# Kernel optimization log

Hardware: AMD Instinct MI355X
Metric: run time of the kernel (lower is better)

The kernel has to match this reference:

```python
import math
import jax, jax.numpy as jnp
import numpy as np

B, S, E, A, H, L, V = 4, 1024, 1024, 64, 16, 2, 32000
EPS = 1e-5
SCALE = math.sqrt(E)  # torch code scales by sqrt(input_dim) = sqrt(embedding_dim)
W_INIT_SCALE = 0.05   # torch.rand is U[0,1); scaled down for numerically sane softmax


def setup_inputs() -> dict:
    key = jax.random.key(0)
    ks = jax.random.split(key, 6)
    return {
        "x": jax.random.randint(ks[0], (B, S), 0, V),
        "emb": jax.random.normal(ks[1], (V, E), dtype=jnp.float32) * 0.02,
        "ln_gamma": jnp.ones((L, E), dtype=jnp.float32),
        "ln_beta": jnp.zeros((L, E), dtype=jnp.float32),
        "Wq": jax.random.uniform(ks[2], (L, H, A, E), dtype=jnp.float32) * W_INIT_SCALE,
        "Wk": jax.random.uniform(ks[3], (L, H, A, E), dtype=jnp.float32) * W_INIT_SCALE,
        "Wv": jax.random.uniform(ks[4], (L, H, E, E), dtype=jnp.float32) * W_INIT_SCALE,
    }


def _attn_layer(h, gamma, beta, wq, wk, wv):
    # h: [B,H,S,E]; LayerNorm over last dim (biased variance, like torch)
    mu = jnp.mean(h, axis=-1, keepdims=True)
    var = jnp.mean(jnp.square(h - mu), axis=-1, keepdims=True)
    hn = (h - mu) * jax.lax.rsqrt(var + EPS) * gamma + beta
    q = jnp.einsum('bhse,hae->bhsa', hn, wq)   # [B,H,S,A]
    k = jnp.einsum('bhse,hae->bhsa', hn, wk)   # [B,H,S,A]
    v = jnp.einsum('bhse,hoe->bhso', hn, wv)   # [B,H,S,E]
    scores = jnp.einsum('bhsa,bhta->bhst', q, k) / SCALE  # [B,H,S,S]
    w = jax.nn.softmax(scores, axis=-1)
    return jnp.einsum('bhst,bhto->bhso', w, v)  # [B,H,S,E]


def reference(x, emb, ln_gamma, ln_beta, Wq, Wk, Wv):
    # embed then replicate across heads: [B,S,E] -> [B,H,S,E]
    h = jnp.broadcast_to(emb[x][:, None, :, :], (B, H, S, E))
    for l in range(L):
        h = _attn_layer(h, ln_gamma[l], ln_beta[l], Wq[l], Wk[l], Wv[l])
    return h
```

## Files before the change

### kernel.cpp

```cpp
#include <hip/hip_runtime.h>

#define B_ 4
#define S_ 1024
#define E_ 1024
#define A_ 64
#define H_ 16
#define L_ 2

static constexpr float LN_EPS = 1e-5f;
static constexpr float INV_SCALE = 1.0f / 32.0f;

typedef __attribute__((ext_vector_type(8))) short bf16x8;
typedef __attribute__((ext_vector_type(4))) float f32x4;

__device__ __forceinline__ unsigned short f2bf(float f) {
  unsigned u = __float_as_uint(f);
  u += 0x7fffu + ((u >> 16) & 1u);
  return (unsigned short)(u >> 16);
}
__device__ __forceinline__ float bf2f(unsigned short s) {
  return __uint_as_float(((unsigned)s) << 16);
}

__device__ __forceinline__ float block_sum256(float v, float* red) {
#pragma unroll
  for (int o = 32; o > 0; o >>= 1) v += __shfl_down(v, o, 64);
  const int lane = threadIdx.x & 63;
  const int w = threadIdx.x >> 6;
  if (lane == 0) red[w] = v;
  __syncthreads();
  if (threadIdx.x == 0) red[0] = red[0] + red[1] + red[2] + red[3];
  __syncthreads();
  float r = red[0];
  __syncthreads();
  return r;
}

__global__ __launch_bounds__(256) void cvt_f32_bf16(const float* __restrict__ in,
                                                    unsigned short* __restrict__ out, long n) {
  long i = ((long)blockIdx.x * 256 + threadIdx.x) * 4;
  const long stride = (long)gridDim.x * 1024;
  for (; i < n; i += stride) {
    float4 v = *(const float4*)(in + i);
    ushort4 o;
    o.x = f2bf(v.x); o.y = f2bf(v.y); o.z = f2bf(v.z); o.w = f2bf(v.w);
    *(ushort4*)(out + i) = o;
  }
}

__global__ __launch_bounds__(256) void cvt_qk_concat(const float* __restrict__ Wq,
                                                     const float* __restrict__ Wk,
                                                     unsigned short* __restrict__ out) {
  const long total = (long)L_ * H_ * 128 * E_;
  long i = ((long)blockIdx.x * 256 + threadIdx.x) * 4;
  const long stride = (long)gridDim.x * 1024;
  for (; i < total; i += stride) {
    const long e = i % E_;
    const long rowhe = i / E_;
    const int row = (int)(rowhe % 128);
    const long lh = rowhe / 128;
    const float* src = (row < 64 ? Wq : Wk) + (lh * 64 + (row & 63)) * E_ + e;
    float4 v = *(const float4*)src;
    ushort4 o;
    o.x = f2bf(v.x); o.y = f2bf(v.y); o.z = f2bf(v.z); o.w = f2bf(v.w);
    *(ushort4*)(out + i) = o;
  }
}

__global__ __launch_bounds__(256) void embed_ln_kernel(
    const int* __restrict__ x, const float* __restrict__ emb,
    const float* __restrict__ gamma, const float* __restrict__ beta,
    unsigned short* __restrict__ out) {
  __shared__ float red[4];
  const int row = blockIdx.x;
  const int tid = threadIdx.x;
  const float* src = emb + (long)x[row] * E_;
  float4 v = *(const float4*)(src + tid * 4);
  const float mean = block_sum256(v.x + v.y + v.z + v.w, red) * (1.f / E_);
  float dx = v.x - mean, dy = v.y - mean, dz = v.z - mean, dw = v.w - mean;
  const float var = block_sum256(dx * dx + dy * dy + dz * dz + dw * dw, red) * (1.f / E_);
  const float rstd = rsqrtf(var + LN_EPS);
  float4 g = *(const float4*)(gamma + tid * 4);
  float4 b = *(const float4*)(beta + tid * 4);
  ushort4 o;
  o.x = f2bf(dx * rstd * g.x + b.x);
  o.y = f2bf(dy * rstd * g.y + b.y);
  o.z = f2bf(dz * rstd * g.z + b.z);
  o.w = f2bf(dw * rstd * g.w + b.w);
  *(ushort4*)(out + (long)row * E_ + tid * 4) = o;
}

__global__ __launch_bounds__(256) void ln_bf16_kernel(
    const unsigned short* __restrict__ h, const float* __restrict__ gamma,
    const float* __restrict__ beta, unsigned short* __restrict__ out) {
  __shared__ float red[4];
  const long row = blockIdx.x;
  const int tid = threadIdx.x;
  ushort4 raw = *(const ushort4*)(h + row * (long)E_ + tid * 4);
  float vx = bf2f(raw.x), vy = bf2f(raw.y), vz = bf2f(raw.z), vw = bf2f(raw.w);
  const float mean = block_sum256(vx + vy + vz + vw, red) * (1.f / E_);
  float dx = vx - mean, dy = vy - mean, dz = vz - mean, dw = vw - mean;
  const float var = block_sum256(dx * dx + dy * dy + dz * dz + dw * dw, red) * (1.f / E_);
  const float rstd = rsqrtf(var + LN_EPS);
  float4 g = *(const float4*)(gamma + tid * 4);
  float4 b = *(const float4*)(beta + tid * 4);
  ushort4 o;
  o.x = f2bf(dx * rstd * g.x + b.x);
  o.y = f2bf(dy * rstd * g.y + b.y);
  o.z = f2bf(dz * rstd * g.z + b.z);
  o.w = f2bf(dw * rstd * g.w + b.w);
  *(ushort4*)(out + row * E_ + tid * 4) = o;
}

__device__ __forceinline__ void gload_lds16(const void* g, void* l) {
  __builtin_amdgcn_global_load_lds((const __attribute__((address_space(1))) void*)g,
                                   (__attribute__((address_space(3))) void*)l, 16, 0, 0);
}

template <int ROWS>
__device__ __forceinline__ void stage_tile(const unsigned short* __restrict__ src, int ldRow,
                                           unsigned short* lds, int tid) {
  const int rb = tid >> 3;
  const int gslot = (tid & 7) ^ (rb & 7);
  const int wbase = (tid >> 6) * 512;
#pragma unroll
  for (int i = 0; i < ROWS / 32; ++i) {
    const unsigned short* g = src + (long)(i * 32 + rb) * ldRow + gslot * 8;
    gload_lds16(g, lds + i * 2048 + wbase);
  }
}

__device__ __forceinline__ bf16x8 lds_frag(const unsigned short* base, int r, int slot) {
  const int byteoff = (r << 7) + ((slot ^ (r & 7)) << 4);
  return *(const bf16x8*)((const char*)base + byteoff);
}

template <int BM, int BN, bool OUT_BF16>
__global__ __launch_bounds__(256) void mfma_gemm_nt(
    const unsigned short* __restrict__ Aall, const unsigned short* __restrict__ Ball,
    void* __restrict__ Call, int M, int N, int K, int lda, int ldb,
    long aSB, long aSH, long bSB, long bSH, int Hn, float alpha) {
  __shared__ unsigned short As[BM * 64];
  __shared__ unsigned short Bs[BN * 64];
  const int batch = blockIdx.z;
  const int bb = batch / Hn, hh = batch % Hn;
  const unsigned short* Ap = Aall + (long)bb * aSB + (long)hh * aSH;
  const unsigned short* Bp = Ball + (long)bb * bSB + (long)hh * bSH;
  const int tid = threadIdx.x;
  const int lane = tid & 63;
  const int wave = tid >> 6;
  const int wr = wave >> 1, wc = wave & 1;
  const int bm = blockIdx.x * BM, bn = blockIdx.y * BN;
  constexpr int FM = BM / 32, FN = BN / 32;

  f32x4 acc[FM][FN];
#pragma unroll
  for (int i = 0; i < FM; ++i)
#pragma unroll
    for (int j = 0; j < FN; ++j) acc[i][j] = (f32x4)(0.f);

  for (int k0 = 0; k0 < K; k0 += 64) {
    stage_tile<BM>(Ap + (long)bm * lda + k0, lda, As, tid);
    stage_tile<BN>(Bp + (long)bn * ldb + k0, ldb, Bs, tid);
    __syncthreads();
#pragma unroll
    for (int kb = 0; kb < 2; ++kb) {
      const int slot = (kb << 2) + (lane >> 4);
      bf16x8 af[FM], bfv[FN];
#pragma unroll
      for (int mi = 0; mi < FM; ++mi)
        af[mi] = lds_frag(As, wr * (BM / 2) + mi * 16 + (lane & 15), slot);
#pragma unroll
      for (int ni = 0; ni < FN; ++ni)
        bfv[ni] = lds_frag(Bs, wc * (BN / 2) + ni * 16 + (lane & 15), slot);
#pragma unroll
      for (int mi = 0; mi < FM; ++mi)
#pragma unroll
        for (int ni = 0; ni < FN; ++ni)
          acc[mi][ni] = __builtin_amdgcn_mfma_f32_16x16x32_bf16(af[mi], bfv[ni], acc[mi][ni], 0, 0, 0);
    }
    __syncthreads();
  }

#pragma unroll
  for (int mi = 0; mi < FM; ++mi) {
    const int row = bm + wr * (BM / 2) + mi * 16 + ((lane >> 4) << 2);
#pragma unroll
    for (int ni = 0; ni < FN; ++ni) {
      const int col = bn + wc * (BN / 2) + ni * 16 + (lane & 15);
#pragma unroll
      for (int r = 0; r < 4; ++r) {
        const float v = acc[mi][ni][r] * alpha;
        const long idx = (long)batch * M * N + (long)(row + r) * N + col;
        if constexpr (OUT_BF16)
          ((unsigned short*)Call)[idx] = f2bf(v);
        else
          ((float*)Call)[idx] = v;
      }
    }
  }
}

__device__ __forceinline__ void stage_unit256(const unsigned short* __restrict__ src, int ldRow,
                                              char* lds_unit, int tid) {
#pragma unroll
  for (int i = 0; i < 2; ++i) {
    const int r = i * 128 + (tid >> 2);
    const int sg = (tid & 3) ^ ((r >> 1) & 3);
    const unsigned short* g = src + (long)r * ldRow + sg * 8;
    gload_lds16(g, lds_unit + i * 8192 + ((tid >> 6) << 10));
  }
}

__device__ __forceinline__ bf16x8 lds_frag256(const char* opbase, int kh, int r, int ss) {
  return *(const bf16x8*)(opbase + kh * 16384 + r * 64 + ((ss ^ ((r >> 1) & 3)) << 4));
}

template <bool OUT_BF16>
__global__ __launch_bounds__(512) void mfma_gemm256_nt(
    const unsigned short* __restrict__ Aall, const unsigned short* __restrict__ Ball,
    void* __restrict__ Call, int M, int N, int K, int lda, int ldb,
    long aSB, long aSH, long bSB, long bSH, int Hn, float alpha) {
  extern __shared__ char lds[];
  const int nx = gridDim.x, ny = gridDim.y;
  const int nwg = nx * ny * gridDim.z;
  int f = blockIdx.x + nx * (blockIdx.y + ny * blockIdx.z);
  if ((nwg & 7) == 0) f = (f & 7) * (nwg >> 3) + (f >> 3);
  const int bx = f % nx;
  const int by = (f / nx) % ny;
  const int batch = f / (nx * ny);

  const int bb = batch / Hn, hh = batch % Hn;
  const unsigned short* Ap = Aall + (long)bb * aSB + (long)hh * aSH + (long)bx * 256 * lda;
  const unsigned short* Bp = Ball + (long)bb * bSB + (long)hh * bSH + (long)by * 256 * ldb;
  const int tid = threadIdx.x;
  const int lane = tid & 63;
  const int w = tid >> 6;
  const int wr = w >> 2, wc = w & 3;
  const int ss = lane >> 4;
  const int ar = lane & 15;

  f32x4 acc[8][4];
#pragma unroll
  for (int i = 0; i < 8; ++i)
#pragma unroll
    for (int j = 0; j < 4; ++j) acc[i][j] = (f32x4)(0.f);

  const int NT = K >> 6;
  stage_unit256(Ap, lda, lds, tid);
  stage_unit256(Ap + 32, lda, lds + 16384, tid);
  stage_unit256(Bp, ldb, lds + 32768, tid);
  stage_unit256(Bp + 32, ldb, lds + 49152, tid);
  __syncthreads();

  for (int t = 0; t < NT; ++t) {
    const char* cur = lds + (t & 1) * 65536;
    char* nxt = lds + ((t + 1) & 1) * 65536;
    if (t + 1 < NT) {
      const unsigned short* An = Ap + (long)(t + 1) * 64;
      const unsigned short* Bn = Bp + (long)(t + 1) * 64;
      stage_unit256(An, lda, nxt, tid);
      stage_unit256(An + 32, lda, nxt + 16384, tid);
      stage_unit256(Bn, ldb, nxt + 32768, tid);
      stage_unit256(Bn + 32, ldb, nxt + 49152, tid);
    }
#pragma unroll
    for (int kh = 0; kh < 2; ++kh) {
      bf16x8 b[4], a[8];
#pragma unroll
      for (int ni = 0; ni < 4; ++ni)
        b[ni] = lds_frag256(cur + 32768, kh, wc * 64 + ni * 16 + ar, ss);
#pragma unroll
      for (int mi = 0; mi < 8; ++mi)
        a[mi] = lds_frag256(cur, kh, wr * 128 + mi * 16 + ar, ss);
#pragma unroll
      for (int mi = 0; mi < 8; ++mi)
#pragma unroll
        for (int ni = 0; ni < 4; ++ni)
          acc[mi][ni] = __builtin_amdgcn_mfma_f32_16x16x32_bf16(a[mi], b[ni], acc[mi][ni], 0, 0, 0);
    }
    __syncthreads();
  }

#pragma unroll
  for (int mi = 0; mi < 8; ++mi) {
    const int row0 = bx * 256 + wr * 128 + mi * 16 + ((lane >> 4) << 2);
#pragma unroll
    for (int ni = 0; ni < 4; ++ni) {
      const int col = by * 256 + wc * 64 + ni * 16 + (lane & 15);
#pragma unroll
      for (int r = 0; r < 4; ++r) {
        const float v = acc[mi][ni][r] * alpha;
        const long idx = (long)batch * M * N + (long)(row0 + r) * N + col;
        if constexpr (OUT_BF16)
          ((unsigned short*)Call)[idx] = f2bf(v);
        else
          ((float*)Call)[idx] = v;
      }
    }
  }
}

__global__ __launch_bounds__(512) void scores_softmax_kernel(
    const unsigned short* __restrict__ qk, unsigned short* __restrict__ sc) {
  extern __shared__ char smem[];
  unsigned short* q_lds = (unsigned short*)smem;
  unsigned short* k_lds = (unsigned short*)(smem + 8192);
  float* redm = (float*)(smem + 8192 + 131072);
  float* reds = redm + 512;

  const int tid = threadIdx.x;
  const int lane = tid & 63;
  const int w = tid >> 6;
  const int batch = blockIdx.z;
  const int bm = blockIdx.x * 64;
  const unsigned short* qbase = qk + (long)batch * S_ * 128 + (long)bm * 128;
  const unsigned short* kbase = qk + (long)batch * S_ * 128 + 64;

  {
    const int r = tid >> 3;
    const int slot = (tid & 7) ^ (r & 7);
    gload_lds16(qbase + (long)r * 128 + slot * 8, (char*)q_lds + w * 1024);
  }
#pragma unroll
  for (int p = 0; p < 16; ++p) {
    const int r = p * 64 + (tid >> 3);
    const int slot = (tid & 7) ^ (r & 7);
    gload_lds16(kbase + (long)r * 128 + slot * 8, (char*)k_lds + p * 8192 + w * 1024);
  }
  __syncthreads();

  const int ss = lane >> 4, ar = lane & 15;
  f32x4 acc[4][8];
#pragma unroll
  for (int i = 0; i < 4; ++i)
#pragma unroll
    for (int j = 0; j < 8; ++j) acc[i][j] = (f32x4)(0.f);

#pragma unroll
  for (int kh = 0; kh < 2; ++kh) {
    bf16x8 a[4];
#pragma unroll
    for (int mi = 0; mi < 4; ++mi)
      a[mi] = lds_frag(q_lds, mi * 16 + ar, kh * 4 + ss);
#pragma unroll
    for (int ni = 0; ni < 8; ++ni) {
      bf16x8 bv = lds_frag(k_lds, w * 128 + ni * 16 + ar, kh * 4 + ss);
#pragma unroll
      for (int mi = 0; mi < 4; ++mi)
        acc[mi][ni] = __builtin_amdgcn_mfma_f32_16x16x32_bf16(a[mi], bv, acc[mi][ni], 0, 0, 0);
    }
  }

#pragma unroll
  for (int mi = 0; mi < 4; ++mi)
#pragma unroll
    for (int ni = 0; ni < 8; ++ni)
#pragma unroll
      for (int r = 0; r < 4; ++r) acc[mi][ni][r] *= INV_SCALE;

  float gmax[4][4];
#pragma unroll
  for (int mi = 0; mi < 4; ++mi)
#pragma unroll
    for (int r = 0; r < 4; ++r) {
      float m = acc[mi][0][r];
#pragma unroll
      for (int ni = 1; ni < 8; ++ni) m = fmaxf(m, acc[mi][ni][r]);
#pragma unroll
      for (int mask = 1; mask < 16; mask <<= 1) m = fmaxf(m, __shfl_xor(m, mask, 64));
      if ((lane & 15) == 0) redm[(mi * 16 + (lane >> 4) * 4 + r) * 8 + w] = m;
      gmax[mi][r] = m;
    }
  __syncthreads();
#pragma unroll
  for (int mi = 0; mi < 4; ++mi)
#pragma unroll
    for (int r = 0; r < 4; ++r) {
      const int row = mi * 16 + (lane >> 4) * 4 + r;
      float g = redm[row * 8];
#pragma unroll
      for (int w2 = 1; w2 < 8; ++w2) g = fmaxf(g, redm[row * 8 + w2]);
      gmax[mi][r] = g;
    }

  float ginv[4][4];
#pragma unroll
  for (int mi = 0; mi < 4; ++mi)
#pragma unroll
    for (int r = 0; r < 4; ++r) {
      float s = 0.f;
#pragma unroll
      for (int ni = 0; ni < 8; ++ni) {
        const float e = __expf(acc[mi][ni][r] - gmax[mi][r]);
        acc[mi][ni][r] = e;
        s += e;
      }
#pragma unroll
      for (int mask = 1; mask < 16; mask <<= 1) s += __shfl_xor(s, mask, 64);
      if ((lane & 15) == 0) reds[(mi * 16 + (lane >> 4) * 4 + r) * 8 + w] = s;
    }
  __syncthreads();
#pragma unroll
  for (int mi = 0; mi < 4; ++mi)
#pragma unroll
    for (int r = 0; r < 4; ++r) {
      const int row = mi * 16 + (lane >> 4) * 4 + r;
      float g = 0.f;
#pragma unroll
      for (int w2 = 0; w2 < 8; ++w2) g += reds[row * 8 + w2];
      ginv[mi][r] = 1.f / g;
    }

  unsigned short* out = sc + (long)batch * S_ * S_;
#pragma unroll
  for (int mi = 0; mi < 4; ++mi)
#pragma unroll
    for (int r = 0; r < 4; ++r) {
      const long row = bm + mi * 16 + (lane >> 4) * 4 + r;
#pragma unroll
      for (int ni = 0; ni < 8; ++ni) {
        const int col = w * 128 + ni * 16 + ar;
        out[row * S_ + col] = f2bf(acc[mi][ni][r] * ginv[mi][r]);
      }
    }
}

extern "C" void kernel_launch(void* const* d_in, const int* in_sizes, int n_in,
                              void* d_out, int out_size, void* d_ws, size_t ws_size,
                              hipStream_t stream) {
  const int* x = (const int*)d_in[0];
  const float* emb = (const float*)d_in[1];
  const float* gamma = (const float*)d_in[2];
  const float* beta = (const float*)d_in[3];
  const float* Wq = (const float*)d_in[4];
  const float* Wk = (const float*)d_in[5];
  const float* Wv = (const float*)d_in[6];
  float* out = (float*)d_out;

  (void)hipFuncSetAttribute(reinterpret_cast<const void*>(&mfma_gemm256_nt<true>),
                            hipFuncAttributeMaxDynamicSharedMemorySize, 131072);
  (void)hipFuncSetAttribute(reinterpret_cast<const void*>(&mfma_gemm256_nt<false>),
                            hipFuncAttributeMaxDynamicSharedMemorySize, 131072);
  (void)hipFuncSetAttribute(reinterpret_cast<const void*>(&scores_softmax_kernel),
                            hipFuncAttributeMaxDynamicSharedMemorySize, 143360);

  const long WQK_N = (long)L_ * H_ * 128 * E_;
  const long WV_N = (long)L_ * H_ * E_ * E_;
  const long HN_N = (long)B_ * H_ * S_ * E_;
  const long QK_N = (long)B_ * H_ * S_ * 128;
  unsigned short* wqk = (unsigned short*)d_ws;
  unsigned short* wv_bf = wqk + WQK_N;
  unsigned short* hn = wv_bf + WV_N;
  unsigned short* qk = hn + HN_N;
  unsigned short* v_t = qk + QK_N;
  unsigned short* sc = v_t + HN_N;
  unsigned short* hid0 = (unsigned short*)d_out;

  const dim3 blk(256), blk512(512);
  const dim3 grid256(4, 4, 64);
  cvt_qk_concat<<<2048, blk, 0, stream>>>(Wq, Wk, wqk);
  cvt_f32_bf16<<<4096, blk, 0, stream>>>(Wv, wv_bf, WV_N);

  for (int l = 0; l < L_; ++l) {
    long hSB, hSH;
    if (l == 0) {
      embed_ln_kernel<<<B_ * S_, blk, 0, stream>>>(x, emb, gamma, beta, hn);
      hSB = (long)S_ * E_; hSH = 0;
    } else {
      ln_bf16_kernel<<<B_ * H_ * S_, blk, 0, stream>>>(
          hid0, gamma + (long)l * E_, beta + (long)l * E_, hn);
      hSB = (long)H_ * S_ * E_; hSH = (long)S_ * E_;
    }
    mfma_gemm_nt<128, 128, true><<<dim3(8, 1, 64), blk, 0, stream>>>(
        hn, wqk + (long)l * H_ * 128 * E_, qk, S_, 128, E_, E_, E_,
        hSB, hSH, 0L, (long)128 * E_, H_, 1.f);
    mfma_gemm256_nt<true><<<grid256, blk512, 131072, stream>>>(
        wv_bf + (long)l * H_ * E_ * E_, hn, v_t, E_, S_, E_, E_, E_,
        0L, (long)E_ * E_, hSB, hSH, H_, 1.f);
    scores_softmax_kernel<<<dim3(16, 1, 64), blk512, 143360, stream>>>(qk, sc);
    if (l == 0) {
      mfma_gemm256_nt<true><<<grid256, blk512, 131072, stream>>>(
          sc, v_t, hid0, S_, E_, S_, S_, S_,
          (long)H_ * S_ * S_, (long)S_ * S_, (long)H_ * E_ * S_, (long)E_ * S_, H_, 1.f);
    } else {
      mfma_gemm256_nt<false><<<grid256, blk512, 131072, stream>>>(
          sc, v_t, out, S_, E_, S_, S_, S_,
          (long)H_ * S_ * S_, (long)S_ * S_, (long)H_ * E_ * S_, (long)E_ * S_, H_, 1.f);
    }
  }
}
```

Measured before the change: 1.031 ms.

## Interleave GEMM loads with MFMA phases and stage bf16 outputs through LDS

The 256x256 GEMM main loop is split into four phases. Each phase issues one quarter of the next tile's global-to-LDS prefetch, waits with explicit vmcnt/lgkmcnt and barriers, and then runs a 4x4 MFMA block at raised wave priority. The goal is to overlap memory traffic with matrix math more evenly and keep fewer fragments live in registers, with launch bounds now requesting two blocks. Both bf16-output paths, the GEMM epilogue and the softmax kernel, now stage results in LDS and write 16-byte vectorized rows instead of scattered 2-byte stores. The cost is extra barriers and hand-tuned wait counts that could be fragile.

New measurement: 1.051 ms. Within noise of the previous version (+1.9%).

```diff
diff --git a/kernel.cpp b/kernel.cpp
--- a/kernel.cpp
+++ b/kernel.cpp
@@ -12,6 +12,8 @@
 
 typedef __attribute__((ext_vector_type(8))) short bf16x8;
 typedef __attribute__((ext_vector_type(4))) float f32x4;
+
+#define SCHED0 __builtin_amdgcn_sched_barrier(0)
 
 __device__ __forceinline__ unsigned short f2bf(float f) {
   unsigned u = __float_as_uint(f);
@@ -217,7 +219,7 @@
 }
 
 template <bool OUT_BF16>
-__global__ __launch_bounds__(512) void mfma_gemm256_nt(
+__global__ __launch_bounds__(512, 2) void mfma_gemm256_nt(
     const unsigned short* __restrict__ Aall, const unsigned short* __restrict__ Ball,
     void* __restrict__ Call, int M, int N, int K, int lda, int ldb,
     long aSB, long aSH, long bSB, long bSH, int Hn, float alpha) {
@@ -248,54 +250,143 @@
 
   const int NT = K >> 6;
   stage_unit256(Ap, lda, lds, tid);
+  stage_unit256(Bp, ldb, lds + 32768, tid);
   stage_unit256(Ap + 32, lda, lds + 16384, tid);
-  stage_unit256(Bp, ldb, lds + 32768, tid);
   stage_unit256(Bp + 32, ldb, lds + 49152, tid);
-  __syncthreads();
+  asm volatile("s_waitcnt vmcnt(4)");
+  SCHED0;
+  __builtin_amdgcn_s_barrier();
+  SCHED0;
 
   for (int t = 0; t < NT; ++t) {
     const char* cur = lds + (t & 1) * 65536;
     char* nxt = lds + ((t + 1) & 1) * 65536;
-    if (t + 1 < NT) {
-      const unsigned short* An = Ap + (long)(t + 1) * 64;
-      const unsigned short* Bn = Bp + (long)(t + 1) * 64;
-      stage_unit256(An, lda, nxt, tid);
+    const unsigned short* An = Ap + (long)(t + 1) * 64;
+    const unsigned short* Bn = Bp + (long)(t + 1) * 64;
+    const bool pf = (t + 1 < NT);
+    bf16x8 a[4], b[4];
+
+#pragma unroll
+    for (int ni = 0; ni < 4; ++ni)
+      b[ni] = lds_frag256(cur + 32768, 0, wc * 64 + ni * 16 + ar, ss);
+#pragma unroll
+    for (int mi = 0; mi < 4; ++mi)
+      a[mi] = lds_frag256(cur, 0, wr * 128 + mi * 16 + ar, ss);
+    if (pf) stage_unit256(An, lda, nxt, tid);
+    asm volatile("s_waitcnt vmcnt(4)");
+    SCHED0;
+    __builtin_amdgcn_s_barrier();
+    asm volatile("s_waitcnt lgkmcnt(0)");
+    SCHED0;
+    __builtin_amdgcn_s_setprio(1);
+#pragma unroll
+    for (int mi = 0; mi < 4; ++mi)
+#pragma unroll
+      for (int ni = 0; ni < 4; ++ni)
+        acc[mi][ni] = __builtin_amdgcn_mfma_f32_16x16x32_bf16(a[mi], b[ni], acc[mi][ni], 0, 0, 0);
+    __builtin_amdgcn_s_setprio(0);
+    __builtin_amdgcn_s_barrier();
+    SCHED0;
+
+#pragma unroll
+    for (int mi = 0; mi < 4; ++mi)
+      a[mi] = lds_frag256(cur, 0, wr * 128 + 64 + mi * 16 + ar, ss);
+    if (pf) stage_unit256(Bn, ldb, nxt + 32768, tid);
+    asm volatile("s_waitcnt vmcnt(4)");
+    SCHED0;
+    __builtin_amdgcn_s_barrier();
+    asm volatile("s_waitcnt lgkmcnt(0)");
+    SCHED0;
+    __builtin_amdgcn_s_setprio(1);
+#pragma unroll
+    for (int mi = 0; mi < 4; ++mi)
+#pragma unroll
+      for (int ni = 0; ni < 4; ++ni)
+        acc[4 + mi][ni] = __builtin_amdgcn_mfma_f32_16x16x32_bf16(a[mi], b[ni], acc[4 + mi][ni], 0, 0, 0);
+    __builtin_amdgcn_s_setprio(0);
+    __builtin_amdgcn_s_barrier();
+    SCHED0;
+
+#pragma unroll
+    for (int ni = 0; ni < 4; ++ni)
+      b[ni] = lds_frag256(cur + 32768, 1, wc * 64 + ni * 16 + ar, ss);
+#pragma unroll
+    for (int mi = 0; mi < 4; ++mi)
+      a[mi] = lds_frag256(cur, 1, wr * 128 + mi * 16 + ar, ss);
+    if (pf) {
       stage_unit256(An + 32, lda, nxt + 16384, tid);
-      stage_unit256(Bn, ldb, nxt + 32768, tid);
-      stage_unit256(Bn + 32, ldb, nxt + 49152, tid);
-    }
-#pragma unroll
-    for (int kh = 0; kh < 2; ++kh) {
-      bf16x8 b[4], a[8];
+      asm volatile("s_waitcnt vmcnt(4)");
+    } else {
+      asm volatile("s_waitcnt vmcnt(0)");
+    }
+    SCHED0;
+    __builtin_amdgcn_s_barrier();
+    asm volatile("s_waitcnt lgkmcnt(0)");
+    SCHED0;
+    __builtin_amdgcn_s_setprio(1);
+#pragma unroll
+    for (int mi = 0; mi < 4; ++mi)
 #pragma unroll
       for (int ni = 0; ni < 4; ++ni)
-        b[ni] = lds_frag256(cur + 32768, kh, wc * 64 + ni * 16 + ar, ss);
-#pragma unroll
-      for (int mi = 0; mi < 8; ++mi)
-        a[mi] = lds_frag256(cur, kh, wr * 128 + mi * 16 + ar, ss);
-#pragma unroll
-      for (int mi = 0; mi < 8; ++mi)
-#pragma unroll
-        for (int ni = 0; ni < 4; ++ni)
-          acc[mi][ni] = __builtin_amdgcn_mfma_f32_16x16x32_bf16(a[mi], b[ni], acc[mi][ni], 0, 0, 0);
-    }
+        acc[mi][ni] = __builtin_amdgcn_mfma_f32_16x16x32_bf16(a[mi], b[ni], acc[mi][ni], 0, 0, 0);
+    __builtin_amdgcn_s_setprio(0);
+    __builtin_amdgcn_s_barrier();
+    SCHED0;
+
+#pragma unroll
+    for (int mi = 0; mi < 4; ++mi)
+      a[mi] = lds_frag256(cur, 1, wr * 128 + 64 + mi * 16 + ar, ss);
+    if (pf) stage_unit256(Bn + 32, ldb, nxt + 49152, tid);
+    asm volatile("s_waitcnt vmcnt(4)");
+    SCHED0;
+    __builtin_amdgcn_s_barrier();
+    asm volatile("s_waitcnt lgkmcnt(0)");
+    SCHED0;
+    __builtin_amdgcn_s_setprio(1);
+#pragma unroll
+    for (int mi = 0; mi < 4; ++mi)
+#pragma unroll
+      for (int ni = 0; ni < 4; ++ni)
+        acc[4 + mi][ni] = __builtin_amdgcn_mfma_f32_16x16x32_bf16(a[mi], b[ni], acc[4 + mi][ni], 0, 0, 0);
+    __builtin_amdgcn_s_setprio(0);
+    __builtin_amdgcn_s_barrier();
+    SCHED0;
+  }
+
+  if constexpr (OUT_BF16) {
     __syncthreads();
-  }
-
-#pragma unroll
-  for (int mi = 0; mi < 8; ++mi) {
-    const int row0 = bx * 256 + wr * 128 + mi * 16 + ((lane >> 4) << 2);
-#pragma unroll
-    for (int ni = 0; ni < 4; ++ni) {
-      const int col = by * 256 + wc * 64 + ni * 16 + (lane & 15);
-#pragma unroll
-      for (int r = 0; r < 4; ++r) {
-        const float v = acc[mi][ni][r] * alpha;
-        const long idx = (long)batch * M * N + (long)(row0 + r) * N + col;
-        if constexpr (OUT_BF16)
-          ((unsigned short*)Call)[idx] = f2bf(v);
-        else
-          ((float*)Call)[idx] = v;
+    char* wbuf = lds + w * 16384;
+#pragma unroll
+    for (int mi = 0; mi < 8; ++mi)
+#pragma unroll
+      for (int ni = 0; ni < 4; ++ni)
+#pragma unroll
+        for (int r = 0; r < 4; ++r) {
+          const int rl = mi * 16 + ((lane >> 4) << 2) + r;
+          const int cl = ni * 16 + ar;
+          *(unsigned short*)(wbuf + rl * 128 + cl * 2) = f2bf(acc[mi][ni][r] * alpha);
+        }
+    unsigned short* Cb = (unsigned short*)Call + (long)batch * M * N;
+    const int R0 = bx * 256 + wr * 128, C0 = by * 256 + wc * 64;
+#pragma unroll
+    for (int it = 0; it < 16; ++it) {
+      const int row = it * 8 + (lane >> 3);
+      const int colc = (lane & 7) * 8;
+      bf16x8 v = *(const bf16x8*)(wbuf + row * 128 + colc * 2);
+      *(bf16x8*)(Cb + (long)(R0 + row) * N + C0 + colc) = v;
+    }
+  } else {
+#pragma unroll
+    for (int mi = 0; mi < 8; ++mi) {
+      const int row0 = bx * 256 + wr * 128 + mi * 16 + ((lane >> 4) << 2);
+#pragma unroll
+      for (int ni = 0; ni < 4; ++ni) {
+        const int col = by * 256 + wc * 64 + ni * 16 + ar;
+#pragma unroll
+        for (int r = 0; r < 4; ++r) {
+          const long idx = (long)batch * M * N + (long)(row0 + r) * N + col;
+          ((float*)Call)[idx] = acc[mi][ni][r] * alpha;
+        }
       }
     }
   }
@@ -412,18 +503,28 @@
       ginv[mi][r] = 1.f / g;
     }
 
-  unsigned short* out = sc + (long)batch * S_ * S_;
+  __syncthreads();
 #pragma unroll
   for (int mi = 0; mi < 4; ++mi)
 #pragma unroll
     for (int r = 0; r < 4; ++r) {
-      const long row = bm + mi * 16 + (lane >> 4) * 4 + r;
+      const int row = mi * 16 + (lane >> 4) * 4 + r;
 #pragma unroll
       for (int ni = 0; ni < 8; ++ni) {
         const int col = w * 128 + ni * 16 + ar;
-        out[row * S_ + col] = f2bf(acc[mi][ni][r] * ginv[mi][r]);
+        *(unsigned short*)((char*)k_lds + row * 2048 + col * 2) =
+            f2bf(acc[mi][ni][r] * ginv[mi][r]);
       }
     }
+  __syncthreads();
+  unsigned short* outp = sc + (long)batch * S_ * S_;
+#pragma unroll
+  for (int it = 0; it < 16; ++it) {
+    const int row = it * 4 + (tid >> 7);
+    const int colc = (tid & 127) * 8;
+    bf16x8 v = *(const bf16x8*)((char*)k_lds + row * 2048 + colc * 2);
+    *(bf16x8*)(outp + (long)(bm + row) * S_ + colc) = v;
+  }
 }
 
 extern "C" void kernel_launch(void* const* d_in, const int* in_sizes, int n_in,
```

## Interleave GEMM prefetch with MFMA phases using fine-grained barriers and priority

Applied to the files above, without the earlier changes.

Splits each K-tile of the 256x256 bf16 GEMM into four phases. Each phase loads half the A fragments, issues one staged global-to-LDS load for the next tile, and runs a block of MFMAs under raised wave priority. Partial vmcnt waits and raw s_barriers replace the single __syncthreads, so global loads overlap with compute. It also sets launch_bounds occupancy to 2 blocks per CU. The risks are more barriers per tile, possible register pressure, and correctness that depends on hand-counted vmcnt values.

Result: faster. 0.9998 ms (-3.1%).

```diff
diff --git a/kernel.cpp b/kernel.cpp
--- a/kernel.cpp
+++ b/kernel.cpp
@@ -217,7 +217,7 @@
 }
 
 template <bool OUT_BF16>
-__global__ __launch_bounds__(512) void mfma_gemm256_nt(
+__global__ __launch_bounds__(512, 2) void mfma_gemm256_nt(
     const unsigned short* __restrict__ Aall, const unsigned short* __restrict__ Ball,
     void* __restrict__ Call, int M, int N, int K, int lda, int ldb,
     long aSB, long aSH, long bSB, long bSH, int Hn, float alpha) {
@@ -248,38 +248,85 @@
 
   const int NT = K >> 6;
   stage_unit256(Ap, lda, lds, tid);
+  stage_unit256(Bp, ldb, lds + 32768, tid);
   stage_unit256(Ap + 32, lda, lds + 16384, tid);
-  stage_unit256(Bp, ldb, lds + 32768, tid);
   stage_unit256(Bp + 32, ldb, lds + 49152, tid);
-  __syncthreads();
+  asm volatile("s_waitcnt vmcnt(4)\n\ts_barrier" ::: "memory");
 
   for (int t = 0; t < NT; ++t) {
     const char* cur = lds + (t & 1) * 65536;
     char* nxt = lds + ((t + 1) & 1) * 65536;
-    if (t + 1 < NT) {
-      const unsigned short* An = Ap + (long)(t + 1) * 64;
-      const unsigned short* Bn = Bp + (long)(t + 1) * 64;
-      stage_unit256(An, lda, nxt, tid);
-      stage_unit256(An + 32, lda, nxt + 16384, tid);
-      stage_unit256(Bn, ldb, nxt + 32768, tid);
+    const unsigned short* An = Ap + (long)(t + 1) * 64;
+    const unsigned short* Bn = Bp + (long)(t + 1) * 64;
+    const bool pf = (t + 1 < NT);
+    bf16x8 a[4], b[4];
+
+#pragma unroll
+    for (int ni = 0; ni < 4; ++ni)
+      b[ni] = lds_frag256(cur + 32768, 0, wc * 64 + ni * 16 + ar, ss);
+#pragma unroll
+    for (int mi = 0; mi < 4; ++mi)
+      a[mi] = lds_frag256(cur, 0, wr * 128 + mi * 16 + ar, ss);
+    if (pf) stage_unit256(An, lda, nxt, tid);
+    asm volatile("s_barrier" ::: "memory");
+    __builtin_amdgcn_s_setprio(1);
+#pragma unroll
+    for (int mi = 0; mi < 4; ++mi)
+#pragma unroll
+      for (int ni = 0; ni < 4; ++ni)
+        acc[mi][ni] = __builtin_amdgcn_mfma_f32_16x16x32_bf16(a[mi], b[ni], acc[mi][ni], 0, 0, 0);
+    __builtin_amdgcn_s_setprio(0);
+    asm volatile("s_barrier" ::: "memory");
+
+#pragma unroll
+    for (int mi = 0; mi < 4; ++mi)
+      a[mi] = lds_frag256(cur, 0, wr * 128 + 64 + mi * 16 + ar, ss);
+    if (pf) stage_unit256(Bn, ldb, nxt + 32768, tid);
+    if (pf) asm volatile("s_waitcnt vmcnt(4)\n\ts_barrier" ::: "memory");
+    else    asm volatile("s_waitcnt vmcnt(0)\n\ts_barrier" ::: "memory");
+    __builtin_amdgcn_s_setprio(1);
+#pragma unroll
+    for (int mi = 0; mi < 4; ++mi)
+#pragma unroll
+      for (int ni = 0; ni < 4; ++ni)
+        acc[4 + mi][ni] = __builtin_amdgcn_mfma_f32_16x16x32_bf16(a[mi], b[ni], acc[4 + mi][ni], 0, 0, 0);
+    __builtin_amdgcn_s_setprio(0);
+    asm volatile("s_barrier" ::: "memory");
+
+#pragma unroll
+    for (int ni = 0; ni < 4; ++ni)
+      b[ni] = lds_frag256(cur + 32768, 1, wc * 64 + ni * 16 + ar, ss);
+#pragma unroll
+    for (int mi = 0; mi < 4; ++mi)
+      a[mi] = lds_frag256(cur, 1, wr * 128 + mi * 16 + ar, ss);
+    if (pf) stage_unit256(An + 32, lda, nxt + 16384, tid);
+    asm volatile("s_barrier" ::: "memory");
+    __builtin_amdgcn_s_setprio(1);
+#pragma unroll
+    for (int mi = 0; mi < 4; ++mi)
+#pragma unroll
+      for (int ni = 0; ni < 4; ++ni)
+        acc[mi][ni] = __builtin_amdgcn_mfma_f32_16x16x32_bf16(a[mi], b[ni], acc[mi][ni], 0, 0, 0);
+    __builtin_amdgcn_s_setprio(0);
+    asm volatile("s_barrier" ::: "memory");
+
+#pragma unroll
+    for (int mi = 0; mi < 4; ++mi)
+      a[mi] = lds_frag256(cur, 1, wr * 128 + 64 + mi * 16 + ar, ss);
+    if (pf) {
       stage_unit256(Bn + 32, ldb, nxt + 49152, tid);
-    }
-#pragma unroll
-    for (int kh = 0; kh < 2; ++kh) {
-      bf16x8 b[4], a[8];
+      asm volatile("s_waitcnt vmcnt(4)\n\ts_barrier" ::: "memory");
+    } else {
+      asm volatile("s_barrier" ::: "memory");
+    }
+    __builtin_amdgcn_s_setprio(1);
+#pragma unroll
+    for (int mi = 0; mi < 4; ++mi)
 #pragma unroll
       for (int ni = 0; ni < 4; ++ni)
-        b[ni] = lds_frag256(cur + 32768, kh, wc * 64 + ni * 16 + ar, ss);
-#pragma unroll
-      for (int mi = 0; mi < 8; ++mi)
-        a[mi] = lds_frag256(cur, kh, wr * 128 + mi * 16 + ar, ss);
-#pragma unroll
-      for (int mi = 0; mi < 8; ++mi)
-#pragma unroll
-        for (int ni = 0; ni < 4; ++ni)
-          acc[mi][ni] = __builtin_amdgcn_mfma_f32_16x16x32_bf16(a[mi], b[ni], acc[mi][ni], 0, 0, 0);
-    }
-    __syncthreads();
+        acc[4 + mi][ni] = __builtin_amdgcn_mfma_f32_16x16x32_bf16(a[mi], b[ni], acc[4 + mi][ni], 0, 0, 0);
+    __builtin_amdgcn_s_setprio(0);
+    asm volatile("s_barrier" ::: "memory");
   }
 
 #pragma unroll
```
